# Kernel optimization log

Hardware: AMD Instinct MI355X
Metric: run time of the kernel (lower is better)

The kernel has to match this reference:

```python
import jax, jax.numpy as jnp
import numpy as np

B, H, W, C = 32, 56, 56, 384
HEADS, WIN, SHIFT = 12, 7, 3
MLP_HID = 4 * C
N = WIN * WIN
EPS = 1e-5


def _rel_pos_index(win):
    ch, cw = np.meshgrid(np.arange(win), np.arange(win), indexing='ij')
    coords = np.stack([ch.ravel(), cw.ravel()])            # (2, N)
    rel = coords[:, :, None] - coords[:, None, :]          # (2, N, N)
    rel = rel.transpose(1, 2, 0).astype(np.int64)
    rel[:, :, 0] += win - 1
    rel[:, :, 1] += win - 1
    rel[:, :, 0] *= 2 * win - 1
    return rel.sum(-1)                                     # (N, N)


def _attn_mask(Hh, Ww, win, shift):
    img = np.zeros((Hh, Ww))
    cnt = 0
    slices = (slice(0, -win), slice(-win, -shift), slice(-shift, None))
    for hs in slices:
        for ws in slices:
            img[hs, ws] = cnt
            cnt += 1
    m = img.reshape(Hh // win, win, Ww // win, win).transpose(0, 2, 1, 3).reshape(-1, win * win)
    am = m[:, None, :] - m[:, :, None]
    return np.where(am != 0, -100.0, 0.0).astype(np.float32)  # (nW, N, N)


REL_IDX = jnp.asarray(_rel_pos_index(WIN))
ATTN_MASK = jnp.asarray(_attn_mask(H, W, WIN, SHIFT))


def setup_inputs() -> dict:
    key = jax.random.key(0)
    ks = jax.random.split(key, 16)
    s = 0.02
    return {
        'x': jax.random.normal(ks[0], (B, H * W, C), jnp.float32),
        'g1': jnp.ones((C,), jnp.float32),
        'b1': jnp.zeros((C,), jnp.float32),
        'qkv_w': jax.random.normal(ks[1], (3 * C, C), jnp.float32) * s,
        'qkv_b': jnp.zeros((3 * C,), jnp.float32),
        'rel_bias': jax.random.normal(ks[2], ((2 * WIN - 1) ** 2, HEADS), jnp.float32) * s,
        'proj_w': jax.random.normal(ks[3], (C, C), jnp.float32) * s,
        'proj_b': jnp.zeros((C,), jnp.float32),
        'g2': jnp.ones((C,), jnp.float32),
        'b2': jnp.zeros((C,), jnp.float32),
        'fc1_w': jax.random.normal(ks[4], (MLP_HID, C), jnp.float32) * s,
        'fc1_b': jnp.zeros((MLP_HID,), jnp.float32),
        'fc2_w': jax.random.normal(ks[5], (C, MLP_HID), jnp.float32) * s,
        'fc2_b': jnp.zeros((C,), jnp.float32),
    }


def _ln(x, g, b):
    m = x.mean(-1, keepdims=True)
    v = jnp.var(x, axis=-1, keepdims=True)
    return (x - m) * jax.lax.rsqrt(v + EPS) * g + b


def reference(x, g1, b1, qkv_w, qkv_b, rel_bias, proj_w, proj_b, g2, b2, fc1_w, fc1_b, fc2_w, fc2_b):
    Bz, L, Cc = x.shape
    hd = Cc // HEADS
    nWh = H // WIN
    shortcut = x

    h = _ln(x, g1, b1).reshape(Bz, H, W, Cc)
    h = jnp.roll(h, (-SHIFT, -SHIFT), axis=(1, 2))
    # window partition -> (Bz*nW, N, C)
    h = h.reshape(Bz, nWh, WIN, nWh, WIN, Cc).transpose(0, 1, 3, 2, 4, 5).reshape(-1, N, Cc)

    qkv = (h @ qkv_w.T + qkv_b).reshape(-1, N, 3, HEADS, hd).transpose(2, 0, 3, 1, 4)
    q, k, v = qkv[0] * (hd ** -0.5), qkv[1], qkv[2]
    attn = jnp.einsum('bhnd,bhmd->bhnm', q, k)  # (Bz*nW, heads, N, N)

    bias = rel_bias[REL_IDX.reshape(-1)].reshape(N, N, HEADS).transpose(2, 0, 1)
    attn = attn + bias[None]

    nW = ATTN_MASK.shape[0]
    attn = attn.reshape(Bz, nW, HEADS, N, N) + ATTN_MASK[None, :, None]
    attn = jax.nn.softmax(attn, axis=-1).reshape(-1, HEADS, N, N)

    out = jnp.einsum('bhnm,bhmd->bhnd', attn, v).transpose(0, 2, 1, 3).reshape(-1, N, Cc)
    out = out @ proj_w.T + proj_b
    # window reverse + unshift
    out = out.reshape(Bz, nWh, nWh, WIN, WIN, Cc).transpose(0, 1, 3, 2, 4, 5).reshape(Bz, H, W, Cc)
    out = jnp.roll(out, (SHIFT, SHIFT), axis=(1, 2)).reshape(Bz, L, Cc)

    x = shortcut + out
    h2 = _ln(x, g2, b2)
    h2 = jax.nn.gelu(h2 @ fc1_w.T + fc1_b, approximate=False)
    h2 = h2 @ fc2_w.T + fc2_b
    return x + h2
```

## Files before the change

kernel.cpp:

```cpp
#include <hip/hip_runtime.h>
#include <hip/hip_bf16.h>
#include <math.h>

#define B_      32
#define H_      56
#define W_      56
#define C_      384
#define HEADS_  12
#define WIN_    7
#define SHIFT_  3
#define NTOK_   49
#define HD_     32
#define T_      100352
#define MLP_    1536
#define TCH_    50176

typedef __bf16 bf16x8 __attribute__((ext_vector_type(8)));
typedef unsigned short u16x8 __attribute__((ext_vector_type(8)));
typedef float  f32x4  __attribute__((ext_vector_type(4)));

__device__ __forceinline__ float bf2f(unsigned short u) {
  union { unsigned int i; float f; } v; v.i = ((unsigned int)u) << 16; return v.f;
}
__device__ __forceinline__ unsigned short f2bf(float f) {
  union { float f; unsigned int i; } v; v.f = f;
  unsigned int x = v.i;
  return (unsigned short)((x + 0x7fffu + ((x >> 16) & 1u)) >> 16);
}
__device__ __forceinline__ float gelu_fast(float x) {
  const float t = 0.79788456f * x * (1.0f + 0.044715f * x * x);
  const float e = __expf(2.0f * t);
  const float th = 1.0f - 2.0f / (e + 1.0f);
  return 0.5f * x * (1.0f + th);
}
__device__ __forceinline__ void gload_lds16(const void* g, void* l) {
  __builtin_amdgcn_global_load_lds(
      (const __attribute__((address_space(1))) void*)g,
      (__attribute__((address_space(3))) void*)l, 16, 0, 0);
}
__device__ __forceinline__ bf16x8 ldg8(const unsigned short* p) {
  u16x8 v = *(const u16x8*)p;
  return __builtin_bit_cast(bf16x8, v);
}

__global__ __launch_bounds__(256)
void wconv_all_kernel(const float* __restrict__ s0, unsigned short* __restrict__ d0,
                      const float* __restrict__ s1, unsigned short* __restrict__ d1,
                      const float* __restrict__ s2, unsigned short* __restrict__ d2,
                      const float* __restrict__ s3, unsigned short* __restrict__ d3) {
  int b = blockIdx.x;
  const float* src; unsigned short* dst;
  if (b < 432)       { src = s0; dst = d0; }
  else if (b < 576)  { src = s1; dst = d1; b -= 432; }
  else if (b < 1152) { src = s2; dst = d2; b -= 576; }
  else               { src = s3; dst = d3; b -= 1152; }
  const int i = (b * 256 + threadIdx.x) * 4;
  const float4 v = *(const float4*)(src + i);
  ushort4 o;
  o.x = f2bf(v.x); o.y = f2bf(v.y); o.z = f2bf(v.z); o.w = f2bf(v.w);
  *(ushort4*)(dst + i) = o;
}

template<int REMAP>
__global__ __launch_bounds__(256)
void ln_kernel(const float* __restrict__ xin, const float* __restrict__ g,
               const float* __restrict__ bb, unsigned short* __restrict__ outbf) {
  const int m = blockIdx.x * 4 + (threadIdx.x >> 6);
  const int lane = threadIdx.x & 63;
  size_t src;
  if (REMAP) {
    int w = m / NTOK_, t = m - w * NTOK_;
    int bz = w >> 6, widx = w & 63;
    int wh = widx >> 3, ww = widx & 7;
    int ih = t / WIN_, iw = t - ih * WIN_;
    int gh = (wh * WIN_ + ih + SHIFT_) % H_;
    int gw = (ww * WIN_ + iw + SHIFT_) % W_;
    src = ((size_t)bz * (H_ * W_) + gh * W_ + gw) * C_;
  } else {
    src = (size_t)m * C_;
  }
  const float* row = xin + src;
  float v[6]; float s = 0.f, s2 = 0.f;
#pragma unroll
  for (int u = 0; u < 6; ++u) {
    v[u] = row[lane + 64 * u];
    s += v[u]; s2 += v[u] * v[u];
  }
#pragma unroll
  for (int off = 32; off; off >>= 1) {
    s  += __shfl_xor(s, off);
    s2 += __shfl_xor(s2, off);
  }
  const float mean = s * (1.0f / C_);
  const float var  = s2 * (1.0f / C_) - mean * mean;
  const float rstd = rsqrtf(var + 1e-5f);
  unsigned short* orow = outbf + (size_t)m * C_;
#pragma unroll
  for (int u = 0; u < 6; ++u) {
    int c = lane + 64 * u;
    orow[c] = f2bf((v[u] - mean) * rstd * g[c] + bb[c]);
  }
}

#define BM 128
#define BN 128
#define BKg 64

template<int EPI>
__global__ __launch_bounds__(256)
void mfma_gemm(const unsigned short* __restrict__ A,
               const unsigned short* __restrict__ Wb,
               const float* __restrict__ bias,
               void* __restrict__ outv,
               const float* __restrict__ resid,
               int M, int Nn, int K) {
  __shared__ unsigned short Al[2][BM * BKg];
  __shared__ unsigned short Bl[2][BM * BKg];
  const int t    = threadIdx.x;
  const int wid  = t >> 6;
  const int lane = t & 63;
  const int wr   = wid >> 1, wc = wid & 1;

  const unsigned int nb = gridDim.x * gridDim.y;
  unsigned int lin = blockIdx.y * gridDim.x + blockIdx.x;
  lin = (lin & 7) * (nb >> 3) + (lin >> 3);
  const int m0 = (int)(lin / gridDim.x) * BM;
  const int n0 = (int)(lin % gridDim.x) * BN;

  f32x4 acc[4][4] = {};

  const int sr8    = lane >> 3;
  const int schunk = (lane & 7) ^ (sr8 & 7);
  const int fr  = lane & 15;
  const int fq  = lane >> 4;

  const int nk = K / BKg;

#define STAGE_(ks, buf)                                                        \
  {                                                                            \
    const int k0_ = (ks) * BKg;                                                \
    _Pragma("unroll")                                                          \
    for (int i = 0; i < 4; ++i) {                                              \
      const int r = i * 32 + wid * 8 + sr8;                                    \
      gload_lds16(A + (size_t)(m0 + r) * K + k0_ + schunk * 8,                 \
                  (void*)(&Al[buf][(i * 32 + wid * 8) * BKg]));                \
      gload_lds16(Wb + (size_t)(n0 + r) * K + k0_ + schunk * 8,                \
                  (void*)(&Bl[buf][(i * 32 + wid * 8) * BKg]));                \
    }                                                                          \
  }

  STAGE_(0, 0);
  int cur = 0;

  for (int ks = 0; ks < nk; ++ks) {
    if (ks + 1 < nk) {
      STAGE_(ks + 1, cur ^ 1);
      asm volatile("s_waitcnt vmcnt(8)" ::: "memory");
    } else {
      asm volatile("s_waitcnt vmcnt(0)" ::: "memory");
    }
    __builtin_amdgcn_sched_barrier(0);
    __builtin_amdgcn_s_barrier();
    __builtin_amdgcn_sched_barrier(0);

    const unsigned short* Ab = &Al[cur][0];
    const unsigned short* Bb = &Bl[cur][0];
#pragma unroll
    for (int kk = 0; kk < 2; ++kk) {
      bf16x8 af[4], bfr[4];
#pragma unroll
      for (int mi = 0; mi < 4; ++mi) {
        const int row = wr * 64 + mi * 16 + fr;
        const int ch  = (kk * 4 + fq) ^ (row & 7);
        af[mi] = *(const bf16x8*)(Ab + (size_t)row * BKg + ch * 8);
      }
#pragma unroll
      for (int ni = 0; ni < 4; ++ni) {
        const int row = wc * 64 + ni * 16 + fr;
        const int ch  = (kk * 4 + fq) ^ (row & 7);
        bfr[ni] = *(const bf16x8*)(Bb + (size_t)row * BKg + ch * 8);
      }
#pragma unroll
      for (int mi = 0; mi < 4; ++mi)
#pragma unroll
        for (int ni = 0; ni < 4; ++ni)
          acc[mi][ni] = __builtin_amdgcn_mfma_f32_16x16x32_bf16(
              af[mi], bfr[ni], acc[mi][ni], 0, 0, 0);
    }

    __builtin_amdgcn_sched_barrier(0);
    __builtin_amdgcn_s_barrier();
    __builtin_amdgcn_sched_barrier(0);
    cur ^= 1;
  }
#undef STAGE_

  const int ecol  = fr;
  const int erow0 = fq * 4;
#pragma unroll
  for (int mi = 0; mi < 4; ++mi) {
#pragma unroll
    for (int r = 0; r < 4; ++r) {
      const int m = m0 + wr * 64 + mi * 16 + erow0 + r;
      size_t dstbase = 0;
      if (EPI == 2) {
        int w = m / NTOK_, tt = m - w * NTOK_;
        int bz = w >> 6, widx = w & 63;
        int wh = widx >> 3, ww = widx & 7;
        int ih = tt / WIN_, iw = tt - ih * WIN_;
        int gh = (wh * WIN_ + ih + SHIFT_) % H_;
        int gw = (ww * WIN_ + iw + SHIFT_) % W_;
        dstbase = ((size_t)bz * (H_ * W_) + gh * W_ + gw) * C_;
      }
#pragma unroll
      for (int ni = 0; ni < 4; ++ni) {
        const int n = n0 + wc * 64 + ni * 16 + ecol;
        float val = acc[mi][ni][r] + bias[n];
        if (EPI == 0) {
          ((unsigned short*)outv)[(size_t)m * Nn + n] = f2bf(val);
        } else if (EPI == 1) {
          ((unsigned short*)outv)[(size_t)m * Nn + n] = f2bf(gelu_fast(val));
        } else if (EPI == 2) {
          ((float*)outv)[dstbase + n] = resid[dstbase + n] + val;
        } else {
          float* o = (float*)outv + (size_t)m * Nn + n;
          *o += val;
        }
      }
    }
  }
}

__global__ __launch_bounds__(64)
void bias_expand_kernel(const float* __restrict__ rel_bias,
                        float* __restrict__ biasx) {
  const int hi = blockIdx.x;
  const int head = hi / NTOK_, i = hi - head * NTOK_;
  const int j = threadIdx.x;
  float v = 0.f;
  if (j < NTOK_) {
    const int ih = i / 7, iw = i - ih * 7;
    const int jh = j / 7, jw = j - jh * 7;
    const int ridx = (ih - jh + 6) * 13 + (iw - jw + 6);
    v = rel_bias[ridx * HEADS_ + head];
  }
  biasx[(size_t)hi * 64 + j] = v;
}

#define AW 2
__global__ __launch_bounds__(64 * AW)
void attn_mfma_kernel(const unsigned short* __restrict__ qkv,
                      const float* __restrict__ biasx,
                      unsigned short* __restrict__ out) {
  __shared__ unsigned short sP[AW][64 * 72];
  __shared__ unsigned short sVT[AW][32 * 72];
  __shared__ float sRI[AW][64];
  const int wid  = threadIdx.x >> 6;
  const int lane = threadIdx.x & 63;
  const int task = blockIdx.x * AW + wid;
  const int w    = task / HEADS_;
  const int head = task - w * HEADS_;
  const int widx = w & 63;
  const int wh = widx >> 3, ww = widx & 7;
  const bool edge = (wh == 7) || (ww == 7);
  const int c  = lane & 15;
  const int fq = lane >> 4;
  unsigned short* Pl = sP[wid];
  unsigned short* Vl = sVT[wid];
  float* Ri = sRI[wid];
  const unsigned short* qw = qkv + (size_t)w * NTOK_ * (3 * C_);

  u16x8 vv[4];
#pragma unroll
  for (int p = 0; p < 4; ++p)
    vv[p] = *(const u16x8*)(qw + (size_t)(p * 16 + c) * (3 * C_) + 2 * C_ + head * HD_ + fq * 8);

  bf16x8 kf[4], qf[4];
#pragma unroll
  for (int nj = 0; nj < 4; ++nj)
    kf[nj] = ldg8(qw + (size_t)(nj * 16 + c) * (3 * C_) + C_ + head * HD_ + fq * 8);
#pragma unroll
  for (int qi = 0; qi < 4; ++qi)
    qf[qi] = ldg8(qw + (size_t)(qi * 16 + c) * (3 * C_) + head * HD_ + fq * 8);

  const f32x4 zero4 = {0.f, 0.f, 0.f, 0.f};
  f32x4 accT[4][4];
#pragma unroll
  for (int nj = 0; nj < 4; ++nj)
#pragma unroll
    for (int qi = 0; qi < 4; ++qi)
      accT[nj][qi] = __builtin_amdgcn_mfma_f32_16x16x32_bf16(kf[nj], qf[qi], zero4, 0, 0, 0);

#pragma unroll
  for (int p = 0; p < 4; ++p)
#pragma unroll
    for (int u = 0; u < 8; ++u)
      Vl[(fq * 8 + u) * 72 + p * 16 + c] = (unsigned short)vv[p][u];

  int lj16[16];
  unsigned jpad = 0;
#pragma unroll
  for (int tt = 0; tt < 16; ++tt) {
    const int j = (tt >> 2) * 16 + fq * 4 + (tt & 3);
    int lj = 0;
    if (j >= NTOK_) jpad |= (1u << tt);
    else if (edge) {
      const int jh = j / 7, jw2 = j - jh * 7;
      const int shj = wh * 7 + jh, swj = ww * 7 + jw2;
      lj = (shj < 49 ? 0 : (shj < 53 ? 1 : 2)) * 3 + (swj < 49 ? 0 : (swj < 53 ? 1 : 2));
    }
    lj16[tt] = lj;
  }

  const float* bh = biasx + (size_t)head * (NTOK_ * 64);
#pragma unroll
  for (int qi = 0; qi < 4; ++qi) {
    const int i  = qi * 16 + c;
    const int ic = i < NTOK_ ? i : 0;
    int li = 0;
    if (edge) {
      const int ih = ic / 7, iw2 = ic - ih * 7;
      const int shi = wh * 7 + ih, swi = ww * 7 + iw2;
      li = (shi < 49 ? 0 : (shi < 53 ? 1 : 2)) * 3 + (swi < 49 ? 0 : (swi < 53 ? 1 : 2));
    }
    float sv[16];
#pragma unroll
    for (int nj = 0; nj < 4; ++nj) {
      const float4 b4 = *(const float4*)(bh + ic * 64 + nj * 16 + fq * 4);
      const float* b4p = (const float*)&b4;
#pragma unroll
      for (int r = 0; r < 4; ++r) {
        const int tt = nj * 4 + r;
        float s = accT[nj][qi][r] * 0.17677669529663687f + b4p[r];
        if (edge && lj16[tt] != li) s -= 100.f;
        if (jpad & (1u << tt)) s = -1e30f;
        sv[tt] = s;
      }
    }
    float mx = sv[0];
#pragma unroll
    for (int tt = 1; tt < 16; ++tt) mx = fmaxf(mx, sv[tt]);
    mx = fmaxf(mx, __shfl_xor(mx, 16));
    mx = fmaxf(mx, __shfl_xor(mx, 32));
    float e[16]; float sm = 0.f;
#pragma unroll
    for (int tt = 0; tt < 16; ++tt) { e[tt] = __expf(sv[tt] - mx); sm += e[tt]; }
    sm += __shfl_xor(sm, 16);
    sm += __shfl_xor(sm, 32);
    if (fq == 0) Ri[i] = 1.0f / sm;
#pragma unroll
    for (int nj = 0; nj < 4; ++nj) {
      ushort4 pk;
      pk.x = f2bf(e[nj * 4 + 0]); pk.y = f2bf(e[nj * 4 + 1]);
      pk.z = f2bf(e[nj * 4 + 2]); pk.w = f2bf(e[nj * 4 + 3]);
      *(ushort4*)(Pl + (size_t)i * 72 + nj * 16 + fq * 4) = pk;
    }
  }

  f32x4 accO[4][2] = {};
#pragma unroll
  for (int kk = 0; kk < 2; ++kk) {
    bf16x8 ap[4], bv[2];
#pragma unroll
    for (int mi = 0; mi < 4; ++mi)
      ap[mi] = __builtin_bit_cast(bf16x8,
          *(const u16x8*)(Pl + (mi * 16 + c) * 72 + kk * 32 + fq * 8));
#pragma unroll
    for (int nd = 0; nd < 2; ++nd)
      bv[nd] = __builtin_bit_cast(bf16x8,
          *(const u16x8*)(Vl + (nd * 16 + c) * 72 + kk * 32 + fq * 8));
#pragma unroll
    for (int mi = 0; mi < 4; ++mi)
#pragma unroll
      for (int nd = 0; nd < 2; ++nd)
        accO[mi][nd] = __builtin_amdgcn_mfma_f32_16x16x32_bf16(ap[mi], bv[nd], accO[mi][nd], 0, 0, 0);
  }

#pragma unroll
  for (int mi = 0; mi < 4; ++mi)
#pragma unroll
    for (int r = 0; r < 4; ++r) {
      const int i = mi * 16 + fq * 4 + r;
      if (i < NTOK_) {
        const float inv = Ri[i];
#pragma unroll
        for (int nd = 0; nd < 2; ++nd)
          out[(size_t)(w * NTOK_ + i) * C_ + head * HD_ + nd * 16 + c] =
              f2bf(accO[mi][nd][r] * inv);
      }
    }
}

extern "C" void kernel_launch(void* const* d_in, const int* in_sizes, int n_in,
                              void* d_out, int out_size, void* d_ws, size_t ws_size,
                              hipStream_t stream) {
  const float* x        = (const float*)d_in[0];
  const float* g1       = (const float*)d_in[1];
  const float* b1       = (const float*)d_in[2];
  const float* qkv_w    = (const float*)d_in[3];
  const float* qkv_b    = (const float*)d_in[4];
  const float* rel_bias = (const float*)d_in[5];
  const float* proj_w   = (const float*)d_in[6];
  const float* proj_b   = (const float*)d_in[7];
  const float* g2       = (const float*)d_in[8];
  const float* b2       = (const float*)d_in[9];
  const float* fc1_w    = (const float*)d_in[10];
  const float* fc1_b    = (const float*)d_in[11];
  const float* fc2_w    = (const float*)d_in[12];
  const float* fc2_b    = (const float*)d_in[13];
  float* out = (float*)d_out;

  char* ws = (char*)d_ws;
  unsigned short* xw   = (unsigned short*)(ws);
  unsigned short* qkvb = (unsigned short*)(ws + 77070336);
  unsigned short* attn_out = xw;
  unsigned short* h2   = xw;
  unsigned short* hidc = qkvb;
  unsigned short* qkv_wb  = (unsigned short*)(ws + 308412416);
  unsigned short* proj_wb = (unsigned short*)(ws + 309297152);
  unsigned short* fc1_wb  = (unsigned short*)(ws + 309592064);
  unsigned short* fc2_wb  = (unsigned short*)(ws + 310771712);
  float*          biasx   = (float*)(ws + 311951360);

  wconv_all_kernel<<<dim3(1728), dim3(256), 0, stream>>>(
      qkv_w, qkv_wb, proj_w, proj_wb, fc1_w, fc1_wb, fc2_w, fc2_wb);
  bias_expand_kernel<<<dim3(HEADS_ * NTOK_), dim3(64), 0, stream>>>(rel_bias, biasx);

  ln_kernel<1><<<dim3(T_ / 4), dim3(256), 0, stream>>>(x, g1, b1, xw);

  mfma_gemm<0><<<dim3(1152 / BN, T_ / BM), dim3(256), 0, stream>>>(
      xw, qkv_wb, qkv_b, (void*)qkvb, nullptr, T_, 1152, 384);

  attn_mfma_kernel<<<dim3((T_ / NTOK_) * HEADS_ / AW), dim3(64 * AW), 0, stream>>>(
      qkvb, biasx, attn_out);

  mfma_gemm<2><<<dim3(384 / BN, T_ / BM), dim3(256), 0, stream>>>(
      attn_out, proj_wb, proj_b, (void*)out, x, T_, 384, 384);

  ln_kernel<0><<<dim3(T_ / 4), dim3(256), 0, stream>>>(out, g2, b2, h2);

  for (int chk = 0; chk < 2; ++chk) {
    const size_t row0 = (size_t)chk * TCH_;
    mfma_gemm<1><<<dim3(MLP_ / BN, TCH_ / BM), dim3(256), 0, stream>>>(
        h2 + row0 * C_, fc1_wb, fc1_b, (void*)hidc, nullptr, TCH_, MLP_, 384);
    mfma_gemm<3><<<dim3(384 / BN, TCH_ / BM), dim3(256), 0, stream>>>(
        hidc, fc2_wb, fc2_b, (void*)(out + row0 * C_), nullptr, TCH_, 384, MLP_);
  }
}
```

Before: 975.2 us.

## Use 256x128 GEMM tiles with 8 waves, single-buffered LDS, and balanced XCD remap

Doubles the GEMM M tile to 256 rows and runs 512 threads (8 waves) per block, so each B tile in LDS is reused by more waves. The double-buffered prefetch pipeline is dropped in favour of a simple load/sync/compute loop with one LDS buffer. The XCD block remap is replaced by a variant that handles grid sizes not divisible by 8. The larger block may raise occupancy per CU, but global-load latency is no longer hidden behind MFMA work. T_/256 and TCH_/256 are not integers (100352/256 = 392, 50176/256 = 196), so tile coverage should be checked.

```diff
diff --git a/kernel.cpp b/kernel.cpp
--- a/kernel.cpp
+++ b/kernel.cpp
@@ -102,30 +102,32 @@
   }
 }
 
-#define BM 128
+#define BM 256
 #define BN 128
 #define BKg 64
 
 template<int EPI>
-__global__ __launch_bounds__(256)
+__global__ __launch_bounds__(512)
 void mfma_gemm(const unsigned short* __restrict__ A,
                const unsigned short* __restrict__ Wb,
                const float* __restrict__ bias,
                void* __restrict__ outv,
                const float* __restrict__ resid,
                int M, int Nn, int K) {
-  __shared__ unsigned short Al[2][BM * BKg];
-  __shared__ unsigned short Bl[2][BM * BKg];
+  __shared__ unsigned short Al[BM * BKg];
+  __shared__ unsigned short Bl[BN * BKg];
   const int t    = threadIdx.x;
   const int wid  = t >> 6;
   const int lane = t & 63;
   const int wr   = wid >> 1, wc = wid & 1;
 
   const unsigned int nb = gridDim.x * gridDim.y;
-  unsigned int lin = blockIdx.y * gridDim.x + blockIdx.x;
-  lin = (lin & 7) * (nb >> 3) + (lin >> 3);
-  const int m0 = (int)(lin / gridDim.x) * BM;
-  const int n0 = (int)(lin % gridDim.x) * BN;
+  const unsigned int lin = blockIdx.y * gridDim.x + blockIdx.x;
+  const unsigned int q = nb >> 3, r = nb & 7;
+  const unsigned int xcd = lin & 7, idx = lin >> 3;
+  const unsigned int wg = (xcd < r ? xcd * (q + 1) : r * (q + 1) + (xcd - r) * q) + idx;
+  const int m0 = (int)(wg / gridDim.x) * BM;
+  const int n0 = (int)(wg % gridDim.x) * BN;
 
   f32x4 acc[4][4] = {};
 
@@ -134,37 +136,22 @@
   const int fr  = lane & 15;
   const int fq  = lane >> 4;
 
-  const int nk = K / BKg;
-
-#define STAGE_(ks, buf)                                                        \
-  {                                                                            \
-    const int k0_ = (ks) * BKg;                                                \
-    _Pragma("unroll")                                                          \
-    for (int i = 0; i < 4; ++i) {                                              \
-      const int r = i * 32 + wid * 8 + sr8;                                    \
-      gload_lds16(A + (size_t)(m0 + r) * K + k0_ + schunk * 8,                 \
-                  (void*)(&Al[buf][(i * 32 + wid * 8) * BKg]));                \
-      gload_lds16(Wb + (size_t)(n0 + r) * K + k0_ + schunk * 8,                \
-                  (void*)(&Bl[buf][(i * 32 + wid * 8) * BKg]));                \
-    }                                                                          \
-  }
-
-  STAGE_(0, 0);
-  int cur = 0;
-
-  for (int ks = 0; ks < nk; ++ks) {
-    if (ks + 1 < nk) {
-      STAGE_(ks + 1, cur ^ 1);
-      asm volatile("s_waitcnt vmcnt(8)" ::: "memory");
-    } else {
-      asm volatile("s_waitcnt vmcnt(0)" ::: "memory");
-    }
-    __builtin_amdgcn_sched_barrier(0);
-    __builtin_amdgcn_s_barrier();
-    __builtin_amdgcn_sched_barrier(0);
-
-    const unsigned short* Ab = &Al[cur][0];
-    const unsigned short* Bb = &Bl[cur][0];
+  for (int k0 = 0; k0 < K; k0 += BKg) {
+    __syncthreads();
+#pragma unroll
+    for (int i = 0; i < 4; ++i) {
+      const int rr = i * 64 + wid * 8 + sr8;
+      gload_lds16(A + (size_t)(m0 + rr) * K + k0 + schunk * 8,
+                  (void*)(Al + (size_t)(i * 64 + wid * 8) * BKg));
+    }
+#pragma unroll
+    for (int i = 0; i < 2; ++i) {
+      const int rr = i * 64 + wid * 8 + sr8;
+      gload_lds16(Wb + (size_t)(n0 + rr) * K + k0 + schunk * 8,
+                  (void*)(Bl + (size_t)(i * 64 + wid * 8) * BKg));
+    }
+    __syncthreads();
+
 #pragma unroll
     for (int kk = 0; kk < 2; ++kk) {
       bf16x8 af[4], bfr[4];
@@ -172,13 +159,13 @@
       for (int mi = 0; mi < 4; ++mi) {
         const int row = wr * 64 + mi * 16 + fr;
         const int ch  = (kk * 4 + fq) ^ (row & 7);
-        af[mi] = *(const bf16x8*)(Ab + (size_t)row * BKg + ch * 8);
+        af[mi] = *(const bf16x8*)(Al + (size_t)row * BKg + ch * 8);
       }
 #pragma unroll
       for (int ni = 0; ni < 4; ++ni) {
         const int row = wc * 64 + ni * 16 + fr;
         const int ch  = (kk * 4 + fq) ^ (row & 7);
-        bfr[ni] = *(const bf16x8*)(Bb + (size_t)row * BKg + ch * 8);
+        bfr[ni] = *(const bf16x8*)(Bl + (size_t)row * BKg + ch * 8);
       }
 #pragma unroll
       for (int mi = 0; mi < 4; ++mi)
@@ -187,21 +174,15 @@
           acc[mi][ni] = __builtin_amdgcn_mfma_f32_16x16x32_bf16(
               af[mi], bfr[ni], acc[mi][ni], 0, 0, 0);
     }
-
-    __builtin_amdgcn_sched_barrier(0);
-    __builtin_amdgcn_s_barrier();
-    __builtin_amdgcn_sched_barrier(0);
-    cur ^= 1;
-  }
-#undef STAGE_
+  }
 
   const int ecol  = fr;
   const int erow0 = fq * 4;
 #pragma unroll
   for (int mi = 0; mi < 4; ++mi) {
 #pragma unroll
-    for (int r = 0; r < 4; ++r) {
-      const int m = m0 + wr * 64 + mi * 16 + erow0 + r;
+    for (int r2 = 0; r2 < 4; ++r2) {
+      const int m = m0 + wr * 64 + mi * 16 + erow0 + r2;
       size_t dstbase = 0;
       if (EPI == 2) {
         int w = m / NTOK_, tt = m - w * NTOK_;
@@ -215,7 +196,7 @@
 #pragma unroll
       for (int ni = 0; ni < 4; ++ni) {
         const int n = n0 + wc * 64 + ni * 16 + ecol;
-        float val = acc[mi][ni][r] + bias[n];
+        float val = acc[mi][ni][r2] + bias[n];
         if (EPI == 0) {
           ((unsigned short*)outv)[(size_t)m * Nn + n] = f2bf(val);
         } else if (EPI == 1) {
@@ -428,22 +409,22 @@
 
   ln_kernel<1><<<dim3(T_ / 4), dim3(256), 0, stream>>>(x, g1, b1, xw);
 
-  mfma_gemm<0><<<dim3(1152 / BN, T_ / BM), dim3(256), 0, stream>>>(
+  mfma_gemm<0><<<dim3(1152 / BN, T_ / BM), dim3(512), 0, stream>>>(
       xw, qkv_wb, qkv_b, (void*)qkvb, nullptr, T_, 1152, 384);
 
   attn_mfma_kernel<<<dim3((T_ / NTOK_) * HEADS_ / AW), dim3(64 * AW), 0, stream>>>(
       qkvb, biasx, attn_out);
 
-  mfma_gemm<2><<<dim3(384 / BN, T_ / BM), dim3(256), 0, stream>>>(
+  mfma_gemm<2><<<dim3(384 / BN, T_ / BM), dim3(512), 0, stream>>>(
       attn_out, proj_wb, proj_b, (void*)out, x, T_, 384, 384);
 
   ln_kernel<0><<<dim3(T_ / 4), dim3(256), 0, stream>>>(out, g2, b2, h2);
 
   for (int chk = 0; chk < 2; ++chk) {
     const size_t row0 = (size_t)chk * TCH_;
-    mfma_gemm<1><<<dim3(MLP_ / BN, TCH_ / BM), dim3(256), 0, stream>>>(
+    mfma_gemm<1><<<dim3(MLP_ / BN, TCH_ / BM), dim3(512), 0, stream>>>(
         h2 + row0 * C_, fc1_wb, fc1_b, (void*)hidc, nullptr, TCH_, MLP_, 384);
-    mfma_gemm<3><<<dim3(384 / BN, TCH_ / BM), dim3(256), 0, stream>>>(
+    mfma_gemm<3><<<dim3(384 / BN, TCH_ / BM), dim3(512), 0, stream>>>(
         hidc, fc2_wb, fc2_b, (void*)(out + row0 * C_), nullptr, TCH_, 384, MLP_);
   }
 }
```

Result: faster. 876.1 us (-10.2%).
